# Kernel tuning notes

Measured on AMD Instinct MI355X. Metric: run time of the kernel, lower is better.

## Reference

```python
import jax, jax.numpy as jnp
import numpy as np

B, S, D, H, DK, DV, DFF, V, L = 2, 1024, 768, 12, 64, 64, 3072, 32000, 4
PAD_ID = 0


def _pos_enc(seq_len, dim):
    # sinusoidal PE: pe[:,0::2]=sin(pos/scale), pe[:,1::2]=cos(pos/scale)
    pos = jnp.arange(seq_len, dtype=jnp.float32)[:, None]
    idx = jnp.arange(dim // 2, dtype=jnp.float32)
    scale = 10000.0 ** (2.0 * idx / dim)
    ang = pos / scale  # [S, D/2]
    return jnp.stack([jnp.sin(ang), jnp.cos(ang)], axis=-1).reshape(seq_len, dim)


def _layernorm(x, s, b):
    m = jnp.mean(x, axis=-1, keepdims=True)
    v = jnp.var(x, axis=-1, keepdims=True)
    return (x - m) / jnp.sqrt(v + 1e-5) * s + b


def setup_inputs() -> dict:
    key = jax.random.key(0)
    ks = jax.random.split(key, 12)
    emb = jax.random.normal(ks[0], (V, D), jnp.float32) * 0.02
    emb = emb.at[PAD_ID].set(0.0)  # padding_idx row zeroed (nn.Embedding padding_idx)
    inp = {
        'x': jax.random.randint(ks[1], (B, S), 0, V),
        'emb': emb,
        'Wq': jax.random.normal(ks[2], (L, D, H * DK), jnp.float32) * 0.02,
        'Wk': jax.random.normal(ks[3], (L, D, H * DK), jnp.float32) * 0.02,
        'Wv': jax.random.normal(ks[4], (L, D, H * DV), jnp.float32) * 0.02,
        'Wo': jax.random.normal(ks[5], (L, H * DV, D), jnp.float32) * 0.02,
        'ln1_s': jnp.ones((L, D), jnp.float32),
        'ln1_b': jnp.zeros((L, D), jnp.float32),
        'W1': jax.random.normal(ks[6], (L, D, DFF), jnp.float32) * 0.02,
        'b1': jnp.zeros((L, DFF), jnp.float32),
        'W2': jax.random.normal(ks[7], (L, DFF, D), jnp.float32) * 0.02,
        'b2': jnp.zeros((L, D), jnp.float32),
        'ln2_s': jnp.ones((L, D), jnp.float32),
        'ln2_b': jnp.zeros((L, D), jnp.float32),
        'lm_W': jax.random.normal(ks[8], (D, V), jnp.float32) * 0.02,
        'lm_b': jnp.zeros((V,), jnp.float32),
    }
    return inp


def reference(x, emb, Wq, Wk, Wv, Wo, ln1_s, ln1_b, W1, b1, W2, b2, ln2_s, ln2_b, lm_W, lm_b):
    Bx, Sx = x.shape
    h = emb[x] + _pos_enc(Sx, D)  # [B, S, D]
    # causal mask from torch.triu(ones, diagonal=0): True on diagonal and above
    # (each token is prevented from attending to itself and future tokens)
    mask = jnp.triu(jnp.ones((Sx, Sx), dtype=bool))
    inv_sqrt_dk = 1.0 / jnp.sqrt(jnp.float32(DK))
    for l in range(L):
        q = (h @ Wq[l]).reshape(Bx, Sx, H, DK).transpose(0, 2, 1, 3)
        k = (h @ Wk[l]).reshape(Bx, Sx, H, DK).transpose(0, 2, 1, 3)
        v = (h @ Wv[l]).reshape(Bx, Sx, H, DV).transpose(0, 2, 1, 3)
        scores = jnp.einsum('bhqd,bhkd->bhqk', q, k) * inv_sqrt_dk
        scores = jnp.where(mask, -jnp.inf, scores)
        # source's custom _stable_softmax: exp(x) / (sum(exp(x)) + 1e-9)
        e = jnp.exp(scores)
        w = e / (jnp.sum(e, axis=-1, keepdims=True) + 1e-9)
        av = jnp.einsum('bhqk,bhkd->bhqd', w, v)
        av = av.transpose(0, 2, 1, 3).reshape(Bx, Sx, H * DV)
        h = _layernorm(h + av @ Wo[l], ln1_s[l], ln1_b[l])
        ff = jax.nn.gelu(h @ W1[l] + b1[l], approximate=False) @ W2[l] + b2[l]
        h = _layernorm(h + ff, ln2_s[l], ln2_b[l])
    return h @ lm_W + lm_b  # [B, S, V] logits
```

## Files before the change

kernel.cpp:

```cpp
#include <hip/hip_runtime.h>
#include <hip/hip_bf16.h>

#define L_LAYERS 4
#define D_MODEL 768
#define SEQ 1024
#define BATCH 2
#define NHEAD 12
#define HDIM 64
#define DFF_DIM 3072
#define VOCAB 32000
#define MROWS (BATCH*SEQ)
#define QKV_PLANE (NHEAD*BATCH*SEQ*HDIM)

typedef __attribute__((ext_vector_type(8))) short bfrag8;
typedef __attribute__((ext_vector_type(4))) float facc4;

#define EPI_PLAIN 0
#define EPI_BIAS 1
#define EPI_GELU_BF16 2
#define EPI_QKV 3

__device__ __forceinline__ void gld_lds16(const __hip_bfloat16* g, __hip_bfloat16* l) {
    __builtin_amdgcn_global_load_lds((const __attribute__((address_space(1))) void*)g,
                                     (__attribute__((address_space(3))) void*)l, 16, 0, 0);
}

__global__ __launch_bounds__(256) void transpose_cast(
    const float* __restrict__ src, __hip_bfloat16* __restrict__ dst,
    const int K, const int N, const long sL, const long dL)
{
    __shared__ float tile[32][33];
    const int z = blockIdx.z;
    const float* s = src + (long)z * sL;
    __hip_bfloat16* d = dst + (long)z * dL;
    const int bx = blockIdx.x * 32;
    const int by = blockIdx.y * 32;
    const int tx = threadIdx.x, ty = threadIdx.y;
    #pragma unroll
    for (int r = 0; r < 4; ++r)
        tile[ty + r*8][tx] = s[(long)(by + ty + r*8) * N + bx + tx];
    __syncthreads();
    #pragma unroll
    for (int r = 0; r < 4; ++r)
        d[(long)(bx + ty + r*8) * K + by + tx] = __float2bfloat16(tile[tx][ty + r*8]);
}

__global__ __launch_bounds__(256) void embed_k(
    const int* __restrict__ xids, const float* __restrict__ emb,
    float* __restrict__ h, __hip_bfloat16* __restrict__ hb)
{
    const int row = blockIdx.x, t = threadIdx.x;
    const int tok = xids[row];
    const int spos = row & (SEQ - 1);
    const long base = (long)row * D_MODEL;
    const long ebase = (long)tok * D_MODEL;
    #pragma unroll
    for (int j = 0; j < 3; ++j) {
        const int d = j*256 + t;
        const int i = d >> 1;
        const float ang = (float)spos * expf(-(float)(2*i) * (9.210340371976184f / 768.0f));
        const float pe = (d & 1) ? cosf(ang) : sinf(ang);
        const float v = emb[ebase + d] + pe;
        h[base + d] = v;
        hb[base + d] = __float2bfloat16(v);
    }
}

__global__ __launch_bounds__(256) void ln_residual(
    float* __restrict__ h, __hip_bfloat16* __restrict__ hb,
    const float* __restrict__ delta,
    const float* __restrict__ sc, const float* __restrict__ bi,
    const int nplanes)
{
    const int row = blockIdx.x, t = threadIdx.x;
    const long base = (long)row * D_MODEL;
    float x[3];
    float s1 = 0.f, s2 = 0.f;
    #pragma unroll
    for (int j = 0; j < 3; ++j) {
        const int d = j*256 + t;
        float v = h[base + d];
        for (int p = 0; p < nplanes; ++p)
            v += delta[(long)p * MROWS * D_MODEL + base + d];
        x[j] = v; s1 += v; s2 += v*v;
    }
    #pragma unroll
    for (int off = 32; off >= 1; off >>= 1) {
        s1 += __shfl_xor(s1, off);
        s2 += __shfl_xor(s2, off);
    }
    __shared__ float r1[4], r2[4];
    const int wv = t >> 6;
    if ((t & 63) == 0) { r1[wv] = s1; r2[wv] = s2; }
    __syncthreads();
    s1 = r1[0] + r1[1] + r1[2] + r1[3];
    s2 = r2[0] + r2[1] + r2[2] + r2[3];
    const float mean = s1 * (1.0f/768.0f);
    const float var  = s2 * (1.0f/768.0f) - mean*mean;
    const float inv  = rsqrtf(var + 1e-5f);
    #pragma unroll
    for (int j = 0; j < 3; ++j) {
        const int d = j*256 + t;
        const float y = (x[j] - mean) * inv * sc[d] + bi[d];
        h[base + d] = y;
        hb[base + d] = __float2bfloat16(y);
    }
}

__global__ __launch_bounds__(256) void gemm_bt(
    const __hip_bfloat16* __restrict__ A,
    const __hip_bfloat16* __restrict__ Bt,
    const float* __restrict__ bias,
    float* __restrict__ outf,
    __hip_bfloat16* __restrict__ outb,
    const int N, const int K, const int epi)
{
    __shared__ __hip_bfloat16 As[2][128*32];
    __shared__ __hip_bfloat16 Bs[2][128*32];
    const int tid = threadIdx.x;
    const int lane = tid & 63, wv = tid >> 6;

    const int nwg  = gridDim.x * gridDim.y;
    const int orig = blockIdx.y * gridDim.x + blockIdx.x;
    const int qq = nwg >> 3, rr = nwg & 7;
    const int xcd = orig & 7, lin = orig >> 3;
    const int wgid = (xcd < rr ? xcd * (qq + 1) : rr * (qq + 1) + (xcd - rr) * qq) + lin;
    const int m8   = wgid & 7;
    const int rest = wgid >> 3;
    const int bni  = rest % gridDim.x;
    const int bmi  = (rest / gridDim.x) * 8 + m8;
    const int bm = bmi * 128, bn = bni * 128;

    const int wm = (wv >> 1) * 64, wn = (wv & 1) * 64;
    const int fr = lane & 15, fq = lane >> 4;

    const int Kc = K / gridDim.z;
    const long zoff = (long)blockIdx.z * Kc;

    facc4 acc[4][4];
    #pragma unroll
    for (int i = 0; i < 4; ++i)
        #pragma unroll
        for (int j = 0; j < 4; ++j) { facc4 z = {0.f,0.f,0.f,0.f}; acc[i][j] = z; }

    const int srow = wv*32 + (lane >> 2);
    const int scol = (lane & 3) * 8;
    const __hip_bfloat16* Ag = A  + (long)(bm + srow) * K + scol + zoff;
    const __hip_bfloat16* Bg = Bt + (long)(bn + srow) * K + scol + zoff;
    __hip_bfloat16* Aw0 = &As[0][wv*1024];
    __hip_bfloat16* Aw1 = &As[1][wv*1024];
    __hip_bfloat16* Bw0 = &Bs[0][wv*1024];
    __hip_bfloat16* Bw1 = &Bs[1][wv*1024];

    const int nt = Kc >> 5;
    gld_lds16(Ag,                 Aw0);
    gld_lds16(Ag + (long)16*K,    Aw0 + 512);
    gld_lds16(Bg,                 Bw0);
    gld_lds16(Bg + (long)16*K,    Bw0 + 512);

    int cur = 0;
    for (int t = 0; t < nt; ++t) {
        __syncthreads();
        if (t + 1 < nt) {
            const int k0 = (t + 1) << 5;
            __hip_bfloat16* aw = cur ? Aw0 : Aw1;
            __hip_bfloat16* bw = cur ? Bw0 : Bw1;
            gld_lds16(Ag + k0,              aw);
            gld_lds16(Ag + k0 + (long)16*K, aw + 512);
            gld_lds16(Bg + k0,              bw);
            gld_lds16(Bg + k0 + (long)16*K, bw + 512);
        }
        const __hip_bfloat16* Ab = cur ? &As[1][0] : &As[0][0];
        const __hip_bfloat16* Bb = cur ? &Bs[1][0] : &Bs[0][0];
        bfrag8 af[4], bf[4];
        #pragma unroll
        for (int i = 0; i < 4; ++i) af[i] = *(const bfrag8*)(Ab + (wm + i*16 + fr)*32 + fq*8);
        #pragma unroll
        for (int j = 0; j < 4; ++j) bf[j] = *(const bfrag8*)(Bb + (wn + j*16 + fr)*32 + fq*8);
        #pragma unroll
        for (int i = 0; i < 4; ++i)
            #pragma unroll
            for (int j = 0; j < 4; ++j)
                acc[i][j] = __builtin_amdgcn_mfma_f32_16x16x32_bf16(af[i], bf[j], acc[i][j], 0, 0, 0);
        cur ^= 1;
    }

    if (epi == EPI_QKV) {
        __hip_bfloat16* qo = outb;
        __hip_bfloat16* ko = outb + QKV_PLANE;
        __hip_bfloat16* vo = outb + 2*QKV_PLANE;
        #pragma unroll
        for (int i = 0; i < 4; ++i) {
            #pragma unroll
            for (int j = 0; j < 4; ++j) {
                const int gn = bn + wn + j*16 + fr;
                const int which = gn / D_MODEL;
                const int nn = gn - which * D_MODEL;
                const int hh = nn >> 6, dd = nn & 63;
                #pragma unroll
                for (int r = 0; r < 4; ++r) {
                    const int gm = bm + wm + i*16 + fq*4 + r;
                    const int bidx = gm >> 10, si = gm & (SEQ-1);
                    const long bh = (long)bidx * NHEAD + hh;
                    const __hip_bfloat16 bv = __float2bfloat16(acc[i][j][r]);
                    if (which == 0)      qo[(bh*SEQ + si)*HDIM + dd] = bv;
                    else if (which == 1) ko[(bh*SEQ + si)*HDIM + dd] = bv;
                    else                 vo[(bh*HDIM + dd)*SEQ + si] = bv;
                }
            }
        }
    } else if (epi == EPI_GELU_BF16) {
        #pragma unroll
        for (int i = 0; i < 4; ++i)
            #pragma unroll
            for (int j = 0; j < 4; ++j) {
                const int gn = bn + wn + j*16 + fr;
                const float bb = bias[gn];
                #pragma unroll
                for (int r = 0; r < 4; ++r) {
                    const int gm = bm + wm + i*16 + fq*4 + r;
                    const float v = acc[i][j][r] + bb;
                    const float g = 0.5f * v * (1.0f + erff(v * 0.70710678118f));
                    outb[(long)gm * N + gn] = __float2bfloat16(g);
                }
            }
    } else if (epi == EPI_BIAS) {
        float* outz = outf + (long)blockIdx.z * (long)(gridDim.y * 128) * N;
        #pragma unroll
        for (int i = 0; i < 4; ++i)
            #pragma unroll
            for (int j = 0; j < 4; ++j) {
                const int gn = bn + wn + j*16 + fr;
                const float bb = (blockIdx.z == 0) ? bias[gn] : 0.f;
                #pragma unroll
                for (int r = 0; r < 4; ++r) {
                    const int gm = bm + wm + i*16 + fq*4 + r;
                    outz[(long)gm * N + gn] = acc[i][j][r] + bb;
                }
            }
    } else {
        float* outz = outf + (long)blockIdx.z * (long)(gridDim.y * 128) * N;
        #pragma unroll
        for (int i = 0; i < 4; ++i)
            #pragma unroll
            for (int j = 0; j < 4; ++j) {
                const int gn = bn + wn + j*16 + fr;
                #pragma unroll
                for (int r = 0; r < 4; ++r) {
                    const int gm = bm + wm + i*16 + fq*4 + r;
                    outz[(long)gm * N + gn] = acc[i][j][r];
                }
            }
    }
}

__global__ __launch_bounds__(512, 2) void gemm256_bias(
    const __hip_bfloat16* __restrict__ A,
    const __hip_bfloat16* __restrict__ Bt,
    const float* __restrict__ bias,
    float* __restrict__ outf,
    const int N, const int K)
{
    __shared__ __hip_bfloat16 ldsA[2][16384];
    __shared__ __hip_bfloat16 ldsB[2][16384];

    const int tid = threadIdx.x;
    const int lane = tid & 63, wv = tid >> 6;
    const int fr = lane & 15, fq = (lane >> 4) & 3;
    const int wr = wv >> 2, wc = wv & 3;

    const int nwg  = gridDim.x;
    const int cpx  = nwg >> 3;
    const int orig = blockIdx.x;
    const int wgid = (orig & 7) * cpx + (orig >> 3);
    const int bm = (wgid & 7) * 256;
    const int bn = (wgid >> 3) * 256;

    const int trow = tid >> 3;
    const int sg   = (tid & 7) ^ (trow & 7);
    const __hip_bfloat16* Ag = A  + (long)(bm + trow) * K + sg * 8;
    const __hip_bfloat16* Bg = Bt + (long)(bn + trow) * K + sg * 8;

#define STAGE_PAIR(m, kt1, buf) do { \
    gld_lds16(Ag + (long)((m)*64) * K + (kt1)*64, &ldsA[buf][(m)*4096 + wv*512]); \
    gld_lds16(Bg + (long)((m)*64) * K + (kt1)*64, &ldsB[buf][(m)*4096 + wv*512]); \
  } while (0)

    facc4 acc[8][4];
    #pragma unroll
    for (int i = 0; i < 8; ++i)
        #pragma unroll
        for (int j = 0; j < 4; ++j) { facc4 z = {0.f,0.f,0.f,0.f}; acc[i][j] = z; }

    const int rowA = wr * 128 + fr;
    const int rowB = wc * 64  + fr;
    const int sx0 = ((fq)     ^ (fr & 7)) * 8;
    const int sx1 = ((4 + fq) ^ (fr & 7)) * 8;

    const int nt = K >> 6;
    STAGE_PAIR(0, 0, 0); STAGE_PAIR(1, 0, 0); STAGE_PAIR(2, 0, 0); STAGE_PAIR(3, 0, 0);

    for (int kt = 0; kt < nt; ++kt) {
        const int p = kt & 1;
        const __hip_bfloat16* Ac = ldsA[p];
        const __hip_bfloat16* Bc = ldsB[p];
        const bool pre = (kt + 1 < nt);

        if (pre) {
            STAGE_PAIR(0, kt+1, p^1);
            asm volatile("s_waitcnt vmcnt(2)" ::: "memory");
        } else {
            asm volatile("s_waitcnt vmcnt(0)" ::: "memory");
        }
        __builtin_amdgcn_s_barrier();
        bfrag8 b[4][2];
        #pragma unroll
        for (int j = 0; j < 4; ++j) {
            b[j][0] = *(const bfrag8*)(Bc + (rowB + j*16)*64 + sx0);
            b[j][1] = *(const bfrag8*)(Bc + (rowB + j*16)*64 + sx1);
        }
        {
            bfrag8 a[2][2];
            #pragma unroll
            for (int ii = 0; ii < 2; ++ii) {
                a[ii][0] = *(const bfrag8*)(Ac + (rowA + ii*16)*64 + sx0);
                a[ii][1] = *(const bfrag8*)(Ac + (rowA + ii*16)*64 + sx1);
            }
            asm volatile("s_waitcnt lgkmcnt(0)" ::: "memory");
            __builtin_amdgcn_sched_barrier(0);
            __builtin_amdgcn_s_setprio(1);
            #pragma unroll
            for (int jj = 0; jj < 4; ++jj)
                #pragma unroll
                for (int ii = 0; ii < 2; ++ii) {
                    acc[ii][jj] = __builtin_amdgcn_mfma_f32_16x16x32_bf16(a[ii][0], b[jj][0], acc[ii][jj], 0, 0, 0);
                    acc[ii][jj] = __builtin_amdgcn_mfma_f32_16x16x32_bf16(a[ii][1], b[jj][1], acc[ii][jj], 0, 0, 0);
                }
            __builtin_amdgcn_s_setprio(0);
        }
        __builtin_amdgcn_s_barrier();

        #pragma unroll
        for (int q = 1; q < 4; ++q) {
            bfrag8 a[2][2];
            #pragma unroll
            for (int ii = 0; ii < 2; ++ii) {
                a[ii][0] = *(const bfrag8*)(Ac + (rowA + (q*2+ii)*16)*64 + sx0);
                a[ii][1] = *(const bfrag8*)(Ac + (rowA + (q*2+ii)*16)*64 + sx1);
            }
            if (pre) {
                if (q == 1)      STAGE_PAIR(1, kt+1, p^1);
                else if (q == 2) STAGE_PAIR(2, kt+1, p^1);
                else             STAGE_PAIR(3, kt+1, p^1);
            }
            __builtin_amdgcn_s_barrier();
            asm volatile("s_waitcnt lgkmcnt(0)" ::: "memory");
            __builtin_amdgcn_sched_barrier(0);
            __builtin_amdgcn_s_setprio(1);
            #pragma unroll
            for (int jj = 0; jj < 4; ++jj)
                #pragma unroll
                for (int ii = 0; ii < 2; ++ii) {
                    acc[q*2+ii][jj] = __builtin_amdgcn_mfma_f32_16x16x32_bf16(a[ii][0], b[jj][0], acc[q*2+ii][jj], 0, 0, 0);
                    acc[q*2+ii][jj] = __builtin_amdgcn_mfma_f32_16x16x32_bf16(a[ii][1], b[jj][1], acc[q*2+ii][jj], 0, 0, 0);
                }
            __builtin_amdgcn_s_setprio(0);
            __builtin_amdgcn_s_barrier();
        }
    }
#undef STAGE_PAIR

    #pragma unroll
    for (int i = 0; i < 8; ++i) {
        const int gm = bm + wr*128 + i*16 + fq*4;
        #pragma unroll
        for (int j = 0; j < 4; ++j) {
            const int gn = bn + wc*64 + j*16 + fr;
            const float bb = bias[gn];
            #pragma unroll
            for (int rr = 0; rr < 4; ++rr)
                outf[(long)(gm + rr) * N + gn] = acc[i][j][rr] + bb;
        }
    }
}

#define KS_STRIDE 80
#define VS_STRIDE 40
#define PS_STRIDE 40
__global__ __launch_bounds__(256) void attn_flash(
    const __hip_bfloat16* __restrict__ Q,
    const __hip_bfloat16* __restrict__ Kp,
    const __hip_bfloat16* __restrict__ Vt,
    __hip_bfloat16* __restrict__ avo)
{
    __shared__ __hip_bfloat16 Ks[32*KS_STRIDE];
    __shared__ __hip_bfloat16 Vs[64*VS_STRIDE];
    __shared__ __hip_bfloat16 Ps[4][16*PS_STRIDE];
    const int tid = threadIdx.x;
    const int lane = tid & 63, wv = tid >> 6;
    const int fr = lane & 15, fq = lane >> 4;
    const int q0 = blockIdx.x * 64;
    const int bh = blockIdx.y;
    const int qrow = q0 + wv*16;

    const __hip_bfloat16* qp = Q + ((long)bh*SEQ + qrow + fr)*HDIM + fq*8;
    const bfrag8 aq0 = *(const bfrag8*)(qp);
    const bfrag8 aq1 = *(const bfrag8*)(qp + 32);

    facc4 accv[4];
    #pragma unroll
    for (int n = 0; n < 4; ++n) { facc4 z = {0.f,0.f,0.f,0.f}; accv[n] = z; }
    float denom[4] = {0.f, 0.f, 0.f, 0.f};

    const __hip_bfloat16* kg = Kp + ((long)bh*SEQ + (tid>>3))*HDIM + (tid&7)*8;
    const __hip_bfloat16* vg = Vt + ((long)bh*HDIM + (tid>>2))*SEQ + (tid&3)*8;
    __hip_bfloat16* ksw = Ks + (tid>>3)*KS_STRIDE + (tid&7)*8;
    __hip_bfloat16* vsw = Vs + (tid>>2)*VS_STRIDE + (tid&3)*8;

    bfrag8 kr = *(const bfrag8*)(kg);
    bfrag8 vr = *(const bfrag8*)(vg);

    const int kend = q0 + 64;
    for (int k0 = 0; k0 < kend; k0 += 32) {
        __syncthreads();
        *(bfrag8*)ksw = kr;
        *(bfrag8*)vsw = vr;
        const long knext = (k0 + 32 < kend) ? (long)(k0 + 32) : (long)k0;
        kr = *(const bfrag8*)(kg + knext * HDIM);
        vr = *(const bfrag8*)(vg + knext);
        __syncthreads();
        #pragma unroll
        for (int t = 0; t < 2; ++t) {
            const int koff = t*16;
            const bfrag8 bk0 = *(const bfrag8*)(Ks + (koff + fr)*KS_STRIDE + fq*8);
            const bfrag8 bk1 = *(const bfrag8*)(Ks + (koff + fr)*KS_STRIDE + 32 + fq*8);
            facc4 sc = {0.f,0.f,0.f,0.f};
            __builtin_amdgcn_s_setprio(1);
            sc = __builtin_amdgcn_mfma_f32_16x16x32_bf16(aq0, bk0, sc, 0, 0, 0);
            sc = __builtin_amdgcn_mfma_f32_16x16x32_bf16(aq1, bk1, sc, 0, 0, 0);
            __builtin_amdgcn_s_setprio(0);
            const int ki = k0 + koff + fr;
            #pragma unroll
            for (int r = 0; r < 4; ++r) {
                const int qi = qrow + fq*4 + r;
                const float e = (ki < qi) ? __expf(sc[r] * 0.125f) : 0.f;
                denom[r] += e;
                Ps[wv][(fq*4 + r)*PS_STRIDE + koff + fr] = __float2bfloat16(e);
            }
        }
        asm volatile("s_waitcnt lgkmcnt(0)" ::: "memory");
        __builtin_amdgcn_sched_barrier(0);
        const bfrag8 ap = *(const bfrag8*)(&Ps[wv][fr*PS_STRIDE + fq*8]);
        __builtin_amdgcn_s_setprio(1);
        #pragma unroll
        for (int n = 0; n < 4; ++n) {
            const bfrag8 bv = *(const bfrag8*)(Vs + (n*16 + fr)*VS_STRIDE + fq*8);
            accv[n] = __builtin_amdgcn_mfma_f32_16x16x32_bf16(ap, bv, accv[n], 0, 0, 0);
        }
        __builtin_amdgcn_s_setprio(0);
    }

    #pragma unroll
    for (int r = 0; r < 4; ++r) {
        #pragma unroll
        for (int off = 1; off < 16; off <<= 1) denom[r] += __shfl_xor(denom[r], off);
    }
    const int bidx = bh / NHEAD, hh = bh % NHEAD;
    #pragma unroll
    for (int n = 0; n < 4; ++n) {
        #pragma unroll
        for (int r = 0; r < 4; ++r) {
            const int qi = qrow + fq*4 + r;
            const int dd = n*16 + fr;
            const float o = accv[n][r] / (denom[r] + 1e-9f);
            avo[((long)(bidx*SEQ + qi))*D_MODEL + hh*HDIM + dd] = __float2bfloat16(o);
        }
    }
}

extern "C" void kernel_launch(void* const* d_in, const int* in_sizes, int n_in,
                              void* d_out, int out_size, void* d_ws, size_t ws_size,
                              hipStream_t stream) {
    const int*   x    = (const int*)d_in[0];
    const float* emb  = (const float*)d_in[1];
    const float* Wq   = (const float*)d_in[2];
    const float* Wk   = (const float*)d_in[3];
    const float* Wv   = (const float*)d_in[4];
    const float* Wo   = (const float*)d_in[5];
    const float* ln1s = (const float*)d_in[6];
    const float* ln1b = (const float*)d_in[7];
    const float* W1   = (const float*)d_in[8];
    const float* b1   = (const float*)d_in[9];
    const float* W2   = (const float*)d_in[10];
    const float* b2   = (const float*)d_in[11];
    const float* ln2s = (const float*)d_in[12];
    const float* ln2b = (const float*)d_in[13];
    const float* lmW  = (const float*)d_in[14];
    const float* lmb  = (const float*)d_in[15];
    float* out = (float*)d_out;

    char* wsp = (char*)d_ws;
    size_t off = 0;
    auto take = [&](size_t bytes) -> char* {
        char* p = wsp + off;
        off += (bytes + 255) & ~(size_t)255;
        return p;
    };
    __hip_bfloat16* wqkvT = (__hip_bfloat16*)take((size_t)L_LAYERS*2304*768*2);
    __hip_bfloat16* woT   = (__hip_bfloat16*)take((size_t)L_LAYERS*768*768*2);
    __hip_bfloat16* w1T   = (__hip_bfloat16*)take((size_t)L_LAYERS*3072*768*2);
    __hip_bfloat16* w2T   = (__hip_bfloat16*)take((size_t)L_LAYERS*768*3072*2);
    __hip_bfloat16* lmT   = (__hip_bfloat16*)take((size_t)VOCAB*768*2);
    float*          hbuf  = (float*)take((size_t)MROWS*D_MODEL*4);
    __hip_bfloat16* hb    = (__hip_bfloat16*)take((size_t)MROWS*D_MODEL*2);
    __hip_bfloat16* qkvb  = (__hip_bfloat16*)take((size_t)3*QKV_PLANE*2);
    __hip_bfloat16* avb   = (__hip_bfloat16*)take((size_t)MROWS*D_MODEL*2);
    __hip_bfloat16* ffb   = (__hip_bfloat16*)take((size_t)MROWS*DFF_DIM*2);
    float*          tmp   = (float*)take((size_t)4*MROWS*D_MODEL*4);

    dim3 tb(32, 8);
    transpose_cast<<<dim3(24,24,4), tb, 0, stream>>>(Wq, wqkvT,              768, 768, (long)768*768, (long)2304*768);
    transpose_cast<<<dim3(24,24,4), tb, 0, stream>>>(Wk, wqkvT + 768*768,    768, 768, (long)768*768, (long)2304*768);
    transpose_cast<<<dim3(24,24,4), tb, 0, stream>>>(Wv, wqkvT + 2*768*768,  768, 768, (long)768*768, (long)2304*768);
    transpose_cast<<<dim3(24,24,4), tb, 0, stream>>>(Wo, woT,                768, 768, (long)768*768, (long)768*768);
    transpose_cast<<<dim3(96,24,4), tb, 0, stream>>>(W1, w1T,                768, 3072, (long)768*3072, (long)3072*768);
    transpose_cast<<<dim3(24,96,4), tb, 0, stream>>>(W2, w2T,                3072, 768, (long)3072*768, (long)768*3072);
    transpose_cast<<<dim3(1000,24,1), tb, 0, stream>>>(lmW, lmT,             768, VOCAB, 0, 0);

    embed_k<<<MROWS, 256, 0, stream>>>(x, emb, hbuf, hb);

    for (int l = 0; l < L_LAYERS; ++l) {
        gemm_bt<<<dim3(18,16), 256, 0, stream>>>(hb, wqkvT + (size_t)l*2304*768, nullptr,
                                                 nullptr, qkvb, 2304, 768, EPI_QKV);
        attn_flash<<<dim3(16,24), 256, 0, stream>>>(qkvb, qkvb + QKV_PLANE, qkvb + 2*QKV_PLANE, avb);
        gemm_bt<<<dim3(6,16,2), 256, 0, stream>>>(avb, woT + (size_t)l*768*768, nullptr,
                                                  tmp, nullptr, 768, 768, EPI_PLAIN);
        ln_residual<<<MROWS, 256, 0, stream>>>(hbuf, hb, tmp, ln1s + l*768, ln1b + l*768, 2);
        gemm_bt<<<dim3(24,16), 256, 0, stream>>>(hb, w1T + (size_t)l*3072*768, b1 + l*DFF_DIM,
                                                 nullptr, ffb, DFF_DIM, 768, EPI_GELU_BF16);
        gemm_bt<<<dim3(6,16,4), 256, 0, stream>>>(ffb, w2T + (size_t)l*768*3072, b2 + l*768,
                                                  tmp, nullptr, 768, DFF_DIM, EPI_BIAS);
        ln_residual<<<MROWS, 256, 0, stream>>>(hbuf, hb, tmp, ln2s + l*768, ln2b + l*768, 4);
    }
    gemm256_bias<<<1000, 512, 0, stream>>>(hb, lmT, lmb, out, VOCAB, 768);
}
```

Before: 1.161 ms.

## Triple-buffer generic GEMM and reorder LM-head GEMM prefetch with finer vmcnt waits

```diff
diff --git a/kernel.cpp b/kernel.cpp
--- a/kernel.cpp
+++ b/kernel.cpp
@@ -115,8 +115,8 @@
     __hip_bfloat16* __restrict__ outb,
     const int N, const int K, const int epi)
 {
-    __shared__ __hip_bfloat16 As[2][128*32];
-    __shared__ __hip_bfloat16 Bs[2][128*32];
+    __shared__ __hip_bfloat16 As[3][128*32];
+    __shared__ __hip_bfloat16 Bs[3][128*32];
     const int tid = threadIdx.x;
     const int lane = tid & 63, wv = tid >> 6;
 
@@ -147,31 +147,28 @@
     const int scol = (lane & 3) * 8;
     const __hip_bfloat16* Ag = A  + (long)(bm + srow) * K + scol + zoff;
     const __hip_bfloat16* Bg = Bt + (long)(bn + srow) * K + scol + zoff;
-    __hip_bfloat16* Aw0 = &As[0][wv*1024];
-    __hip_bfloat16* Aw1 = &As[1][wv*1024];
-    __hip_bfloat16* Bw0 = &Bs[0][wv*1024];
-    __hip_bfloat16* Bw1 = &Bs[1][wv*1024];
+
+    auto stage = [&](int tk, int buf) {
+        const long k0 = (long)tk << 5;
+        gld_lds16(Ag + k0,              &As[buf][wv*1024]);
+        gld_lds16(Ag + k0 + (long)16*K, &As[buf][wv*1024 + 512]);
+        gld_lds16(Bg + k0,              &Bs[buf][wv*1024]);
+        gld_lds16(Bg + k0 + (long)16*K, &Bs[buf][wv*1024 + 512]);
+    };
 
     const int nt = Kc >> 5;
-    gld_lds16(Ag,                 Aw0);
-    gld_lds16(Ag + (long)16*K,    Aw0 + 512);
-    gld_lds16(Bg,                 Bw0);
-    gld_lds16(Bg + (long)16*K,    Bw0 + 512);
-
-    int cur = 0;
+    stage(0, 0);
+    if (nt > 1) stage(1, 1);
+    asm volatile("s_waitcnt vmcnt(4)" ::: "memory");
+    __builtin_amdgcn_s_barrier();
+
+    int rb = 0, sb = 2;
     for (int t = 0; t < nt; ++t) {
-        __syncthreads();
-        if (t + 1 < nt) {
-            const int k0 = (t + 1) << 5;
-            __hip_bfloat16* aw = cur ? Aw0 : Aw1;
-            __hip_bfloat16* bw = cur ? Bw0 : Bw1;
-            gld_lds16(Ag + k0,              aw);
-            gld_lds16(Ag + k0 + (long)16*K, aw + 512);
-            gld_lds16(Bg + k0,              bw);
-            gld_lds16(Bg + k0 + (long)16*K, bw + 512);
-        }
-        const __hip_bfloat16* Ab = cur ? &As[1][0] : &As[0][0];
-        const __hip_bfloat16* Bb = cur ? &Bs[1][0] : &Bs[0][0];
+        const bool pre = (t + 2 < nt);
+        if (pre) stage(t + 2, sb);
+
+        const __hip_bfloat16* Ab = &As[rb][0];
+        const __hip_bfloat16* Bb = &Bs[rb][0];
         bfrag8 af[4], bf[4];
         #pragma unroll
         for (int i = 0; i < 4; ++i) af[i] = *(const bfrag8*)(Ab + (wm + i*16 + fr)*32 + fq*8);
@@ -182,7 +179,14 @@
             #pragma unroll
             for (int j = 0; j < 4; ++j)
                 acc[i][j] = __builtin_amdgcn_mfma_f32_16x16x32_bf16(af[i], bf[j], acc[i][j], 0, 0, 0);
-        cur ^= 1;
+
+        asm volatile("s_waitcnt lgkmcnt(0)" ::: "memory");
+        if (pre) { asm volatile("s_waitcnt vmcnt(4)" ::: "memory"); }
+        else     { asm volatile("s_waitcnt vmcnt(0)" ::: "memory"); }
+        __builtin_amdgcn_s_barrier();
+
+        rb = (rb == 2) ? 0 : rb + 1;
+        sb = (sb == 2) ? 0 : sb + 1;
     }
 
     if (epi == EPI_QKV) {
@@ -281,10 +285,8 @@
     const __hip_bfloat16* Ag = A  + (long)(bm + trow) * K + sg * 8;
     const __hip_bfloat16* Bg = Bt + (long)(bn + trow) * K + sg * 8;
 
-#define STAGE_PAIR(m, kt1, buf) do { \
-    gld_lds16(Ag + (long)((m)*64) * K + (kt1)*64, &ldsA[buf][(m)*4096 + wv*512]); \
-    gld_lds16(Bg + (long)((m)*64) * K + (kt1)*64, &ldsB[buf][(m)*4096 + wv*512]); \
-  } while (0)
+#define SA_G(m, kt1, buf) gld_lds16(Ag + (long)((m)*64) * K + (kt1)*64, &ldsA[buf][(m)*4096 + wv*512])
+#define SB_G(m, kt1, buf) gld_lds16(Bg + (long)((m)*64) * K + (kt1)*64, &ldsB[buf][(m)*4096 + wv*512])
 
     facc4 acc[8][4];
     #pragma unroll
@@ -298,19 +300,21 @@
     const int sx1 = ((4 + fq) ^ (fr & 7)) * 8;
 
     const int nt = K >> 6;
-    STAGE_PAIR(0, 0, 0); STAGE_PAIR(1, 0, 0); STAGE_PAIR(2, 0, 0); STAGE_PAIR(3, 0, 0);
+    SB_G(0,0,0); SB_G(1,0,0); SB_G(2,0,0); SB_G(3,0,0);
+    SA_G(0,0,0); SA_G(2,0,0); SA_G(1,0,0); SA_G(3,0,0);
 
     for (int kt = 0; kt < nt; ++kt) {
         const int p = kt & 1;
         const __hip_bfloat16* Ac = ldsA[p];
         const __hip_bfloat16* Bc = ldsB[p];
+        const int nb = p ^ 1;
         const bool pre = (kt + 1 < nt);
 
         if (pre) {
-            STAGE_PAIR(0, kt+1, p^1);
+            SB_G(0, kt+1, nb); SB_G(1, kt+1, nb); SB_G(2, kt+1, nb); SB_G(3, kt+1, nb);
+            asm volatile("s_waitcnt vmcnt(6)" ::: "memory");
+        } else {
             asm volatile("s_waitcnt vmcnt(2)" ::: "memory");
-        } else {
-            asm volatile("s_waitcnt vmcnt(0)" ::: "memory");
         }
         __builtin_amdgcn_s_barrier();
         bfrag8 b[4][2];
@@ -340,19 +344,14 @@
         }
         __builtin_amdgcn_s_barrier();
 
-        #pragma unroll
-        for (int q = 1; q < 4; ++q) {
+        {
             bfrag8 a[2][2];
             #pragma unroll
             for (int ii = 0; ii < 2; ++ii) {
-                a[ii][0] = *(const bfrag8*)(Ac + (rowA + (q*2+ii)*16)*64 + sx0);
-                a[ii][1] = *(const bfrag8*)(Ac + (rowA + (q*2+ii)*16)*64 + sx1);
-            }
-            if (pre) {
-                if (q == 1)      STAGE_PAIR(1, kt+1, p^1);
-                else if (q == 2) STAGE_PAIR(2, kt+1, p^1);
-                else             STAGE_PAIR(3, kt+1, p^1);
-            }
+                a[ii][0] = *(const bfrag8*)(Ac + (rowA + (2+ii)*16)*64 + sx0);
+                a[ii][1] = *(const bfrag8*)(Ac + (rowA + (2+ii)*16)*64 + sx1);
+            }
+            if (pre) { SA_G(0, kt+1, nb); SA_G(2, kt+1, nb); }
             __builtin_amdgcn_s_barrier();
             asm volatile("s_waitcnt lgkmcnt(0)" ::: "memory");
             __builtin_amdgcn_sched_barrier(0);
@@ -361,14 +360,65 @@
             for (int jj = 0; jj < 4; ++jj)
                 #pragma unroll
                 for (int ii = 0; ii < 2; ++ii) {
-                    acc[q*2+ii][jj] = __builtin_amdgcn_mfma_f32_16x16x32_bf16(a[ii][0], b[jj][0], acc[q*2+ii][jj], 0, 0, 0);
-                    acc[q*2+ii][jj] = __builtin_amdgcn_mfma_f32_16x16x32_bf16(a[ii][1], b[jj][1], acc[q*2+ii][jj], 0, 0, 0);
+                    acc[2+ii][jj] = __builtin_amdgcn_mfma_f32_16x16x32_bf16(a[ii][0], b[jj][0], acc[2+ii][jj], 0, 0, 0);
+                    acc[2+ii][jj] = __builtin_amdgcn_mfma_f32_16x16x32_bf16(a[ii][1], b[jj][1], acc[2+ii][jj], 0, 0, 0);
                 }
             __builtin_amdgcn_s_setprio(0);
+        }
+        __builtin_amdgcn_s_barrier();
+
+        if (pre) {
+            SA_G(1, kt+1, nb); SA_G(3, kt+1, nb);
+            asm volatile("s_waitcnt vmcnt(8)" ::: "memory");
+        } else {
+            asm volatile("s_waitcnt vmcnt(0)" ::: "memory");
+        }
+        __builtin_amdgcn_s_barrier();
+        {
+            bfrag8 a[2][2];
+            #pragma unroll
+            for (int ii = 0; ii < 2; ++ii) {
+                a[ii][0] = *(const bfrag8*)(Ac + (rowA + (4+ii)*16)*64 + sx0);
+                a[ii][1] = *(const bfrag8*)(Ac + (rowA + (4+ii)*16)*64 + sx1);
+            }
+            asm volatile("s_waitcnt lgkmcnt(0)" ::: "memory");
+            __builtin_amdgcn_sched_barrier(0);
+            __builtin_amdgcn_s_setprio(1);
+            #pragma unroll
+            for (int jj = 0; jj < 4; ++jj)
+                #pragma unroll
+                for (int ii = 0; ii < 2; ++ii) {
+                    acc[4+ii][jj] = __builtin_amdgcn_mfma_f32_16x16x32_bf16(a[ii][0], b[jj][0], acc[4+ii][jj], 0, 0, 0);
+                    acc[4+ii][jj] = __builtin_amdgcn_mfma_f32_16x16x32_bf16(a[ii][1], b[jj][1], acc[4+ii][jj], 0, 0, 0);
+                }
+            __builtin_amdgcn_s_setprio(0);
+        }
+        __builtin_amdgcn_s_barrier();
+
+        {
+            bfrag8 a[2][2];
+            #pragma unroll
+            for (int ii = 0; ii < 2; ++ii) {
+                a[ii][0] = *(const bfrag8*)(Ac + (rowA + (6+ii)*16)*64 + sx0);
+                a[ii][1] = *(const bfrag8*)(Ac + (rowA + (6+ii)*16)*64 + sx1);
+            }
             __builtin_amdgcn_s_barrier();
-        }
-    }
-#undef STAGE_PAIR
+            asm volatile("s_waitcnt lgkmcnt(0)" ::: "memory");
+            __builtin_amdgcn_sched_barrier(0);
+            __builtin_amdgcn_s_setprio(1);
+            #pragma unroll
+            for (int jj = 0; jj < 4; ++jj)
+                #pragma unroll
+                for (int ii = 0; ii < 2; ++ii) {
+                    acc[6+ii][jj] = __builtin_amdgcn_mfma_f32_16x16x32_bf16(a[ii][0], b[jj][0], acc[6+ii][jj], 0, 0, 0);
+                    acc[6+ii][jj] = __builtin_amdgcn_mfma_f32_16x16x32_bf16(a[ii][1], b[jj][1], acc[6+ii][jj], 0, 0, 0);
+                }
+            __builtin_amdgcn_s_setprio(0);
+        }
+        __builtin_amdgcn_s_barrier();
+    }
+#undef SA_G
+#undef SB_G
 
     #pragma unroll
     for (int i = 0; i < 8; ++i) {
```

Result: slower. 1.214 ms (+4.6%).
